# Kernel optimization log

Hardware: AMD Instinct MI355X
Metric: run time of the kernel (lower is better)

Reference implementation:

```python
import jax, jax.numpy as jnp
import numpy as np

N_NODES = 50000

def _gcn_conv(x, W, b, src, dst, norm, n_nodes):
    # PyG GCNConv: linear transform, then normalized scatter-add aggregation.
    h = x @ W                                   # [N, out]
    msg = h[src] * norm[:, None]                # [E', out] gather + scale
    out = jax.ops.segment_sum(msg, dst, num_segments=n_nodes)  # scatter-add
    return out + b

def _norm_edges(edge_index, n_nodes):
    # Add self loops, compute symmetric deg^{-1/2} normalization (PyG default).
    loops = jnp.arange(n_nodes, dtype=edge_index.dtype)
    src = jnp.concatenate([edge_index[0], loops])
    dst = jnp.concatenate([edge_index[1], loops])
    deg = jax.ops.segment_sum(jnp.ones_like(dst, dtype=jnp.float32), dst,
                              num_segments=n_nodes)
    dinv = jnp.where(deg > 0, jax.lax.rsqrt(deg), 0.0)
    norm = dinv[src] * dinv[dst]
    return src, dst, norm

def setup_inputs() -> dict:
    key = jax.random.key(0)
    k1, k2, k3, k4, k5 = jax.random.split(key, 5)
    d_in, d_hid, d_out = 128, 96, 64
    x = jax.random.normal(k1, (N_NODES, d_in), dtype=jnp.float32)
    edge_index = jax.random.randint(k2, (2, 800000), 0, N_NODES, dtype=jnp.int32)
    W1 = jax.random.normal(k3, (d_in, d_hid), dtype=jnp.float32) / np.sqrt(d_in)
    b1 = jnp.zeros((d_hid,), dtype=jnp.float32)
    W2 = jax.random.normal(k4, (d_hid, d_out), dtype=jnp.float32) / np.sqrt(d_hid)
    b2 = jnp.zeros((d_out,), dtype=jnp.float32)
    return {"x": x, "edge_index": edge_index, "W1": W1, "b1": b1, "W2": W2, "b2": b2}

def reference(x, edge_index, W1, b1, W2, b2):
    n = x.shape[0]
    src, dst, norm = _norm_edges(edge_index, n)
    h = jax.nn.relu(_gcn_conv(x, W1, b1, src, dst, norm, n))
    # dropout is identity in eval mode
    out = jax.nn.relu(_gcn_conv(h, W2, b2, src, dst, norm, n))
    return out
```

## Files before the change

kernel.cpp:

```cpp
#include <hip/hip_runtime.h>

#define D_IN 128
#define D_HID 96
#define D_OUT 64
#define CHUNK 4096

__global__ void deg_kernel(const int* __restrict__ dst, int* __restrict__ deg, int E) {
    int e0 = (blockIdx.x * blockDim.x + threadIdx.x) * 4;
    if (e0 + 3 < E) {
        int4 d = *(const int4*)&dst[e0];
        atomicAdd(&deg[d.x], 1);
        atomicAdd(&deg[d.y], 1);
        atomicAdd(&deg[d.z], 1);
        atomicAdd(&deg[d.w], 1);
    } else {
        for (int j = 0; j < 4; ++j) {
            int e = e0 + j;
            if (e < E) atomicAdd(&deg[dst[e]], 1);
        }
    }
}

__global__ void scanA_kernel(const int* __restrict__ deg, int* __restrict__ partial, int n) {
    __shared__ int wsum[16];
    const int tid = threadIdx.x, lane = tid & 63, wid = tid >> 6;
    int i0 = blockIdx.x * CHUNK + tid * 4;
    int s = 0;
    if (i0 + 3 < n) {
        int4 v = *(const int4*)&deg[i0];
        s = v.x + v.y + v.z + v.w;
    } else {
        for (int j = 0; j < 4; ++j) if (i0 + j < n) s += deg[i0 + j];
    }
    for (int off = 32; off; off >>= 1) s += __shfl_down(s, off);
    if (lane == 0) wsum[wid] = s;
    __syncthreads();
    if (tid == 0) {
        int t = 0;
        for (int w = 0; w < 16; ++w) t += wsum[w];
        partial[blockIdx.x] = t;
    }
}

__global__ void scanB_kernel(const int* __restrict__ partial, int* __restrict__ offs, int nb) {
    int lane = threadIdx.x;
    int v = (lane < nb) ? partial[lane] : 0;
    int s = v;
    for (int off = 1; off < 64; off <<= 1) {
        int t = __shfl_up(s, off);
        if (lane >= off) s += t;
    }
    if (lane < nb) offs[lane] = s - v;
}

__global__ void scanC_kernel(const int* __restrict__ deg, const int* __restrict__ offs,
                             int* __restrict__ row_ptr, int* __restrict__ cursor,
                             float* __restrict__ dinv, int n) {
    __shared__ int wsum[16];
    const int tid = threadIdx.x, lane = tid & 63, wid = tid >> 6;
    const int base = offs[blockIdx.x];
    int i0 = blockIdx.x * CHUNK + tid * 4;
    int v0 = (i0 + 0 < n) ? deg[i0 + 0] : 0;
    int v1 = (i0 + 1 < n) ? deg[i0 + 1] : 0;
    int v2 = (i0 + 2 < n) ? deg[i0 + 2] : 0;
    int v3 = (i0 + 3 < n) ? deg[i0 + 3] : 0;
    int p0 = v0, p1 = p0 + v1, p2 = p1 + v2, p3 = p2 + v3;
    int tsum = p3;
    for (int off = 1; off < 64; off <<= 1) {
        int t = __shfl_up(tsum, off);
        if (lane >= off) tsum += t;
    }
    if (lane == 63) wsum[wid] = tsum;
    __syncthreads();
    if (wid == 0) {
        int w = (lane < 16) ? wsum[lane] : 0;
        for (int off = 1; off < 16; off <<= 1) {
            int t = __shfl_up(w, off);
            if (lane >= off) w += t;
        }
        if (lane < 16) wsum[lane] = w;
    }
    __syncthreads();
    int texcl = base + (wid ? wsum[wid - 1] : 0) + tsum - p3;
    int e0 = texcl, e1 = texcl + p0, e2 = texcl + p1, e3 = texcl + p2;
    if (i0 + 0 < n) { row_ptr[i0+0] = e0; cursor[i0+0] = e0; dinv[i0+0] = rsqrtf((float)v0 + 1.0f); }
    if (i0 + 1 < n) { row_ptr[i0+1] = e1; cursor[i0+1] = e1; dinv[i0+1] = rsqrtf((float)v1 + 1.0f); }
    if (i0 + 2 < n) { row_ptr[i0+2] = e2; cursor[i0+2] = e2; dinv[i0+2] = rsqrtf((float)v2 + 1.0f); }
    if (i0 + 3 < n) { row_ptr[i0+3] = e3; cursor[i0+3] = e3; dinv[i0+3] = rsqrtf((float)v3 + 1.0f); }
}

__global__ void fill_kernel(const int* __restrict__ src, const int* __restrict__ dst,
                            int* __restrict__ cursor, unsigned short* __restrict__ srcIdx, int E) {
    int e0 = (blockIdx.x * blockDim.x + threadIdx.x) * 4;
    if (e0 + 3 < E) {
        int4 d = *(const int4*)&dst[e0];
        int4 s = *(const int4*)&src[e0];
        int p0 = atomicAdd(&cursor[d.x], 1);
        int p1 = atomicAdd(&cursor[d.y], 1);
        int p2 = atomicAdd(&cursor[d.z], 1);
        int p3 = atomicAdd(&cursor[d.w], 1);
        srcIdx[p0] = (unsigned short)s.x;
        srcIdx[p1] = (unsigned short)s.y;
        srcIdx[p2] = (unsigned short)s.z;
        srcIdx[p3] = (unsigned short)s.w;
    } else {
        for (int j = 0; j < 4; ++j) {
            int e = e0 + j;
            if (e < E) {
                int pos = atomicAdd(&cursor[dst[e]], 1);
                srcIdx[pos] = (unsigned short)src[e];
            }
        }
    }
}

template <int K, int C, int BM>
__global__ void gemm_tiled_kernel(const float* __restrict__ X, const float* __restrict__ W,
                                  const float* __restrict__ dinv, float* __restrict__ H, int n) {
    constexpr int KT = 32;
    constexpr int TX = C / 4;
    constexpr int TY = BM / 4;
    constexpr int NTH = TX * TY;
    constexpr int WS = C + 4;
    constexpr int XS = KT + 4;
    __shared__ float Wl[KT * WS];
    __shared__ float Xl[BM * XS];

    const int tx = threadIdx.x, ty = threadIdx.y;
    const int tlin = ty * TX + tx;
    const int r0 = blockIdx.x * BM;
    const int row0 = ty * 4;

    float4 acc0 = {0,0,0,0}, acc1 = {0,0,0,0}, acc2 = {0,0,0,0}, acc3 = {0,0,0,0};

    for (int kt0 = 0; kt0 < K; kt0 += KT) {
        for (int q = tlin; q < KT * (C / 4); q += NTH) {
            int k = q / (C / 4), cq = q % (C / 4);
            *(float4*)&Wl[k * WS + cq * 4] = *(const float4*)&W[(long)(kt0 + k) * C + cq * 4];
        }
        for (int q = tlin; q < BM * (KT / 4); q += NTH) {
            int r = q / (KT / 4), kq = q % (KT / 4);
            int gr = r0 + r; if (gr >= n) gr = n - 1;
            *(float4*)&Xl[r * XS + kq * 4] = *(const float4*)&X[(long)gr * K + kt0 + kq * 4];
        }
        __syncthreads();
#pragma unroll 4
        for (int k = 0; k < KT; ++k) {
            float4 w = *(const float4*)&Wl[k * WS + tx * 4];
            float x0 = Xl[(row0 + 0) * XS + k];
            float x1 = Xl[(row0 + 1) * XS + k];
            float x2 = Xl[(row0 + 2) * XS + k];
            float x3 = Xl[(row0 + 3) * XS + k];
            acc0.x = fmaf(x0, w.x, acc0.x); acc0.y = fmaf(x0, w.y, acc0.y);
            acc0.z = fmaf(x0, w.z, acc0.z); acc0.w = fmaf(x0, w.w, acc0.w);
            acc1.x = fmaf(x1, w.x, acc1.x); acc1.y = fmaf(x1, w.y, acc1.y);
            acc1.z = fmaf(x1, w.z, acc1.z); acc1.w = fmaf(x1, w.w, acc1.w);
            acc2.x = fmaf(x2, w.x, acc2.x); acc2.y = fmaf(x2, w.y, acc2.y);
            acc2.z = fmaf(x2, w.z, acc2.z); acc2.w = fmaf(x2, w.w, acc2.w);
            acc3.x = fmaf(x3, w.x, acc3.x); acc3.y = fmaf(x3, w.y, acc3.y);
            acc3.z = fmaf(x3, w.z, acc3.z); acc3.w = fmaf(x3, w.w, acc3.w);
        }
        __syncthreads();
    }

    float4 a[4] = {acc0, acc1, acc2, acc3};
#pragma unroll
    for (int i = 0; i < 4; ++i) {
        int row = r0 + row0 + i;
        if (row < n) {
            float di = dinv[row];
            float4 o = {a[i].x * di, a[i].y * di, a[i].z * di, a[i].w * di};
            *(float4*)&H[(long)row * C + tx * 4] = o;
        }
    }
}

template <int C, int NY>
__global__ void agg4_kernel(const int* __restrict__ row_ptr, const int* __restrict__ deg,
                            const unsigned short* __restrict__ srcIdx, const float* __restrict__ hs,
                            const float* __restrict__ dinv, const float* __restrict__ b,
                            float* __restrict__ out, int n) {
    int tx = threadIdx.x;
    int d = blockIdx.x * NY + threadIdx.y;
    if (d >= n) return;
    int start = row_ptr[d];
    int cnt   = deg[d];
    float4 acc = *(const float4*)&hs[(long)d * C + tx * 4];
    int k = 0;
    for (; k + 1 < cnt; k += 2) {
        int s0 = srcIdx[start + k];
        int s1 = srcIdx[start + k + 1];
        float4 v0 = *(const float4*)&hs[(long)s0 * C + tx * 4];
        float4 v1 = *(const float4*)&hs[(long)s1 * C + tx * 4];
        acc.x += v0.x + v1.x; acc.y += v0.y + v1.y;
        acc.z += v0.z + v1.z; acc.w += v0.w + v1.w;
    }
    if (k < cnt) {
        float4 v = *(const float4*)&hs[(long)srcIdx[start + k] * C + tx * 4];
        acc.x += v.x; acc.y += v.y; acc.z += v.z; acc.w += v.w;
    }
    float di = dinv[d];
    const float4 bb = *(const float4*)&b[tx * 4];
    float4 o;
    o.x = fmaxf(fmaf(di, acc.x, bb.x), 0.f);
    o.y = fmaxf(fmaf(di, acc.y, bb.y), 0.f);
    o.z = fmaxf(fmaf(di, acc.z, bb.z), 0.f);
    o.w = fmaxf(fmaf(di, acc.w, bb.w), 0.f);
    *(float4*)&out[(long)d * C + tx * 4] = o;
}

extern "C" void kernel_launch(void* const* d_in, const int* in_sizes, int n_in,
                              void* d_out, int out_size, void* d_ws, size_t ws_size,
                              hipStream_t stream) {
    const float* x  = (const float*)d_in[0];
    const int*   ei = (const int*)d_in[1];
    const float* W1 = (const float*)d_in[2];
    const float* b1 = (const float*)d_in[3];
    const float* W2 = (const float*)d_in[4];
    const float* b2 = (const float*)d_in[5];
    float* out = (float*)d_out;

    const int n = in_sizes[0] / D_IN;
    const int E = in_sizes[1] / 2;
    const int* srcp = ei;
    const int* dstp = ei + E;

    char* ws = (char*)d_ws;
    float* dinv   = (float*)(ws);
    int*   deg    = (int*)  (ws + (256u << 10));
    int*   rowp   = (int*)  (ws + (512u << 10));
    int*   cursor = (int*)  (ws + (768u << 10));
    int*   partial= (int*)  (ws + (968u << 10));
    int*   offs   = (int*)  (ws + (996u << 10));
    unsigned short* srcIdx = (unsigned short*)(ws + (1u << 20));
    float* h1s    = (float*)(ws + (5u << 20));
    float* act1   = (float*)(ws + (25u << 20));
    float* g2s    = h1s;

    hipMemsetAsync(deg, 0, (size_t)n * sizeof(int), stream);

    const int nb = (n + CHUNK - 1) / CHUNK;

    deg_kernel<<<(E / 4 + 255) / 256, 256, 0, stream>>>(dstp, deg, E);
    scanA_kernel<<<nb, 1024, 0, stream>>>(deg, partial, n);
    scanB_kernel<<<1, 64, 0, stream>>>(partial, offs, nb);
    scanC_kernel<<<nb, 1024, 0, stream>>>(deg, offs, rowp, cursor, dinv, n);
    fill_kernel<<<(E / 4 + 255) / 256, 256, 0, stream>>>(srcp, dstp, cursor, srcIdx, E);

    const int BM = 64;
    const int nblk = (n + BM - 1) / BM;

    {
        dim3 blk(D_HID / 4, BM / 4);
        gemm_tiled_kernel<D_IN, D_HID, BM><<<nblk, blk, 0, stream>>>(x, W1, dinv, h1s, n);
        dim3 ablk(D_HID / 4, 8);
        agg4_kernel<D_HID, 8><<<(n + 7) / 8, ablk, 0, stream>>>(rowp, deg, srcIdx, h1s, dinv, b1, act1, n);
    }

    {
        dim3 blk(D_OUT / 4, BM / 4);
        gemm_tiled_kernel<D_HID, D_OUT, BM><<<nblk, blk, 0, stream>>>(act1, W2, dinv, g2s, n);
        dim3 ablk(D_OUT / 4, 16);
        agg4_kernel<D_OUT, 16><<<(n + 15) / 16, ablk, 0, stream>>>(rowp, deg, srcIdx, g2s, dinv, b2, out, n);
    }
}
```

Baseline: 285.7 us.

## Fuse first GEMM with degree counting and move source scaling into aggregation

The layer-1 GEMM no longer depends on dinv, so it is launched together with the degree-count atomics in a single grid, with extra blocks doing the degree work alongside the GEMM tiles. The source-side deg^-1/2 scaling for layer 1 moves into the aggregation kernel as a per-edge dinv gather and FMA. The aggregation loop is also unrolled to four neighbours to keep more gathers in flight. This removes one launch and lets the GEMM overlap the atomics, at the cost of an extra random dinv load per edge in the first aggregation.

Measured after the change: 268.2 us. 1.07x faster.

```diff
diff --git a/kernel.cpp b/kernel.cpp
--- a/kernel.cpp
+++ b/kernel.cpp
@@ -5,19 +5,79 @@
 #define D_OUT 64
 #define CHUNK 4096
 
-__global__ void deg_kernel(const int* __restrict__ dst, int* __restrict__ deg, int E) {
-    int e0 = (blockIdx.x * blockDim.x + threadIdx.x) * 4;
-    if (e0 + 3 < E) {
-        int4 d = *(const int4*)&dst[e0];
-        atomicAdd(&deg[d.x], 1);
-        atomicAdd(&deg[d.y], 1);
-        atomicAdd(&deg[d.z], 1);
-        atomicAdd(&deg[d.w], 1);
-    } else {
-        for (int j = 0; j < 4; ++j) {
-            int e = e0 + j;
-            if (e < E) atomicAdd(&deg[dst[e]], 1);
-        }
+template <int K, int C, int BM>
+__global__ void gemm1_deg_kernel(const float* __restrict__ X, const float* __restrict__ W,
+                                 float* __restrict__ H, int n, int nblkGemm,
+                                 const int* __restrict__ dst, int* __restrict__ deg, int E) {
+    constexpr int KT = 32;
+    constexpr int TX = C / 4;
+    constexpr int TY = BM / 4;
+    constexpr int NTH = TX * TY;
+    constexpr int WS = C + 4;
+    constexpr int XS = KT + 4;
+    __shared__ float Wl[KT * WS];
+    __shared__ float Xl[BM * XS];
+
+    const int tx = threadIdx.x, ty = threadIdx.y;
+    const int tlin = ty * TX + tx;
+
+    if (blockIdx.x >= nblkGemm) {
+        int e0 = ((blockIdx.x - nblkGemm) * NTH + tlin) * 4;
+        if (e0 + 3 < E) {
+            int4 d = *(const int4*)&dst[e0];
+            atomicAdd(&deg[d.x], 1);
+            atomicAdd(&deg[d.y], 1);
+            atomicAdd(&deg[d.z], 1);
+            atomicAdd(&deg[d.w], 1);
+        } else {
+            for (int j = 0; j < 4; ++j) {
+                int e = e0 + j;
+                if (e < E) atomicAdd(&deg[dst[e]], 1);
+            }
+        }
+        return;
+    }
+
+    const int r0 = blockIdx.x * BM;
+    const int row0 = ty * 4;
+
+    float4 acc0 = {0,0,0,0}, acc1 = {0,0,0,0}, acc2 = {0,0,0,0}, acc3 = {0,0,0,0};
+
+    for (int kt0 = 0; kt0 < K; kt0 += KT) {
+        for (int q = tlin; q < KT * (C / 4); q += NTH) {
+            int k = q / (C / 4), cq = q % (C / 4);
+            *(float4*)&Wl[k * WS + cq * 4] = *(const float4*)&W[(long)(kt0 + k) * C + cq * 4];
+        }
+        for (int q = tlin; q < BM * (KT / 4); q += NTH) {
+            int r = q / (KT / 4), kq = q % (KT / 4);
+            int gr = r0 + r; if (gr >= n) gr = n - 1;
+            *(float4*)&Xl[r * XS + kq * 4] = *(const float4*)&X[(long)gr * K + kt0 + kq * 4];
+        }
+        __syncthreads();
+#pragma unroll 4
+        for (int k = 0; k < KT; ++k) {
+            float4 w = *(const float4*)&Wl[k * WS + tx * 4];
+            float x0 = Xl[(row0 + 0) * XS + k];
+            float x1 = Xl[(row0 + 1) * XS + k];
+            float x2 = Xl[(row0 + 2) * XS + k];
+            float x3 = Xl[(row0 + 3) * XS + k];
+            acc0.x = fmaf(x0, w.x, acc0.x); acc0.y = fmaf(x0, w.y, acc0.y);
+            acc0.z = fmaf(x0, w.z, acc0.z); acc0.w = fmaf(x0, w.w, acc0.w);
+            acc1.x = fmaf(x1, w.x, acc1.x); acc1.y = fmaf(x1, w.y, acc1.y);
+            acc1.z = fmaf(x1, w.z, acc1.z); acc1.w = fmaf(x1, w.w, acc1.w);
+            acc2.x = fmaf(x2, w.x, acc2.x); acc2.y = fmaf(x2, w.y, acc2.y);
+            acc2.z = fmaf(x2, w.z, acc2.z); acc2.w = fmaf(x2, w.w, acc2.w);
+            acc3.x = fmaf(x3, w.x, acc3.x); acc3.y = fmaf(x3, w.y, acc3.y);
+            acc3.z = fmaf(x3, w.z, acc3.z); acc3.w = fmaf(x3, w.w, acc3.w);
+        }
+        __syncthreads();
+    }
+
+    float4 a[4] = {acc0, acc1, acc2, acc3};
+#pragma unroll
+    for (int i = 0; i < 4; ++i) {
+        int row = r0 + row0 + i;
+        if (row < n) *(float4*)&H[(long)row * C + tx * 4] = a[i];
     }
 }
 
@@ -175,7 +235,7 @@
     }
 }
 
-template <int C, int NY>
+template <int C, int NY, bool SCALE_SRC>
 __global__ void agg4_kernel(const int* __restrict__ row_ptr, const int* __restrict__ deg,
                             const unsigned short* __restrict__ srcIdx, const float* __restrict__ hs,
                             const float* __restrict__ dinv, const float* __restrict__ b,
@@ -185,21 +245,47 @@
     if (d >= n) return;
     int start = row_ptr[d];
     int cnt   = deg[d];
+    float di  = dinv[d];
     float4 acc = *(const float4*)&hs[(long)d * C + tx * 4];
+    if (SCALE_SRC) { acc.x *= di; acc.y *= di; acc.z *= di; acc.w *= di; }
     int k = 0;
-    for (; k + 1 < cnt; k += 2) {
-        int s0 = srcIdx[start + k];
+    for (; k + 3 < cnt; k += 4) {
+        int s0 = srcIdx[start + k + 0];
         int s1 = srcIdx[start + k + 1];
+        int s2 = srcIdx[start + k + 2];
+        int s3 = srcIdx[start + k + 3];
         float4 v0 = *(const float4*)&hs[(long)s0 * C + tx * 4];
         float4 v1 = *(const float4*)&hs[(long)s1 * C + tx * 4];
-        acc.x += v0.x + v1.x; acc.y += v0.y + v1.y;
-        acc.z += v0.z + v1.z; acc.w += v0.w + v1.w;
-    }
-    if (k < cnt) {
-        float4 v = *(const float4*)&hs[(long)srcIdx[start + k] * C + tx * 4];
-        acc.x += v.x; acc.y += v.y; acc.z += v.z; acc.w += v.w;
-    }
-    float di = dinv[d];
+        float4 v2 = *(const float4*)&hs[(long)s2 * C + tx * 4];
+        float4 v3 = *(const float4*)&hs[(long)s3 * C + tx * 4];
+        if (SCALE_SRC) {
+            float n0 = dinv[s0], n1 = dinv[s1], n2 = dinv[s2], n3 = dinv[s3];
+            acc.x = fmaf(v0.x, n0, acc.x); acc.y = fmaf(v0.y, n0, acc.y);
+            acc.z = fmaf(v0.z, n0, acc.z); acc.w = fmaf(v0.w, n0, acc.w);
+            acc.x = fmaf(v1.x, n1, acc.x); acc.y = fmaf(v1.y, n1, acc.y);
+            acc.z = fmaf(v1.z, n1, acc.z); acc.w = fmaf(v1.w, n1, acc.w);
+            acc.x = fmaf(v2.x, n2, acc.x); acc.y = fmaf(v2.y, n2, acc.y);
+            acc.z = fmaf(v2.z, n2, acc.z); acc.w = fmaf(v2.w, n2, acc.w);
+            acc.x = fmaf(v3.x, n3, acc.x); acc.y = fmaf(v3.y, n3, acc.y);
+            acc.z = fmaf(v3.z, n3, acc.z); acc.w = fmaf(v3.w, n3, acc.w);
+        } else {
+            acc.x += v0.x + v1.x + v2.x + v3.x;
+            acc.y += v0.y + v1.y + v2.y + v3.y;
+            acc.z += v0.z + v1.z + v2.z + v3.z;
+            acc.w += v0.w + v1.w + v2.w + v3.w;
+        }
+    }
+    for (; k < cnt; ++k) {
+        int s = srcIdx[start + k];
+        float4 v = *(const float4*)&hs[(long)s * C + tx * 4];
+        if (SCALE_SRC) {
+            float nm = dinv[s];
+            acc.x = fmaf(v.x, nm, acc.x); acc.y = fmaf(v.y, nm, acc.y);
+            acc.z = fmaf(v.z, nm, acc.z); acc.w = fmaf(v.w, nm, acc.w);
+        } else {
+            acc.x += v.x; acc.y += v.y; acc.z += v.z; acc.w += v.w;
+        }
+    }
     const float4 bb = *(const float4*)&b[tx * 4];
     float4 o;
     o.x = fmaxf(fmaf(di, acc.x, bb.x), 0.f);
@@ -233,34 +319,39 @@
     int*   partial= (int*)  (ws + (968u << 10));
     int*   offs   = (int*)  (ws + (996u << 10));
     unsigned short* srcIdx = (unsigned short*)(ws + (1u << 20));
-    float* h1s    = (float*)(ws + (5u << 20));
+    float* h1     = (float*)(ws + (5u << 20));
     float* act1   = (float*)(ws + (25u << 20));
-    float* g2s    = h1s;
+    float* g2s    = h1;
 
     hipMemsetAsync(deg, 0, (size_t)n * sizeof(int), stream);
 
     const int nb = (n + CHUNK - 1) / CHUNK;
-
-    deg_kernel<<<(E / 4 + 255) / 256, 256, 0, stream>>>(dstp, deg, E);
+    const int BM = 64;
+    const int nblk = (n + BM - 1) / BM;
+
+    {
+        const int degBlocks = (E / 4 + 383) / 384;
+        dim3 blk(D_HID / 4, BM / 4);
+        gemm1_deg_kernel<D_IN, D_HID, BM><<<nblk + degBlocks, blk, 0, stream>>>(
+            x, W1, h1, n, nblk, dstp, deg, E);
+    }
+
     scanA_kernel<<<nb, 1024, 0, stream>>>(deg, partial, n);
     scanB_kernel<<<1, 64, 0, stream>>>(partial, offs, nb);
     scanC_kernel<<<nb, 1024, 0, stream>>>(deg, offs, rowp, cursor, dinv, n);
     fill_kernel<<<(E / 4 + 255) / 256, 256, 0, stream>>>(srcp, dstp, cursor, srcIdx, E);
 
-    const int BM = 64;
-    const int nblk = (n + BM - 1) / BM;
-
     {
-        dim3 blk(D_HID / 4, BM / 4);
-        gemm_tiled_kernel<D_IN, D_HID, BM><<<nblk, blk, 0, stream>>>(x, W1, dinv, h1s, n);
         dim3 ablk(D_HID / 4, 8);
-        agg4_kernel<D_HID, 8><<<(n + 7) / 8, ablk, 0, stream>>>(rowp, deg, srcIdx, h1s, dinv, b1, act1, n);
+        agg4_kernel<D_HID, 8, true><<<(n + 7) / 8, ablk, 0, stream>>>(
+            rowp, deg, srcIdx, h1, dinv, b1, act1, n);
     }
 
     {
         dim3 blk(D_OUT / 4, BM / 4);
         gemm_tiled_kernel<D_HID, D_OUT, BM><<<nblk, blk, 0, stream>>>(act1, W2, dinv, g2s, n);
         dim3 ablk(D_OUT / 4, 16);
-        agg4_kernel<D_OUT, 16><<<(n + 15) / 16, ablk, 0, stream>>>(rowp, deg, srcIdx, g2s, dinv, b2, out, n);
-    }
-}
+        agg4_kernel<D_OUT, 16, false><<<(n + 15) / 16, ablk, 0, stream>>>(
+            rowp, deg, srcIdx, g2s, dinv, b2, out, n);
+    }
+}
```
